# Optimization experiments

Hardware: AMD Instinct MI355X
Metric: run time of the kernel (lower is better)

Reference implementation:

```python
import jax, jax.numpy as jnp
from jax import lax
import numpy as np

B, T, NAG, MTASK = 8, 32, 50, 100  # batch, timesteps, n agents, m tasks
MTOP, NNB, L, H = 10, 10, 5, 512   # M top tasks, N neighbors (must equal M), L, hidden_dim
IN_DIM = NNB * MTOP * L + NNB * MTASK + NNB + NNB * MTOP  # 1610


def setup_inputs() -> dict:
    key = jax.random.key(0)
    ks = jax.random.split(key, 8)
    return {
        "beta": jax.random.normal(ks[0], (B, T, NAG, MTASK, L), dtype=jnp.float32),
        "actions_onehot": jax.random.uniform(ks[1], (B, T, NAG, MTASK), dtype=jnp.float32),
        "power_states": jax.random.normal(ks[2], (B, T, NAG), dtype=jnp.float32),
        "prev_assigns": jax.random.randint(ks[3], (B, T, NAG), 0, MTASK, dtype=jnp.int32),
        "W1": jax.random.normal(ks[4], (IN_DIM, H), dtype=jnp.float32) * 0.02,
        "b1": jnp.zeros((H,), jnp.float32),
        "W2": jax.random.normal(ks[5], (H, H), dtype=jnp.float32) * 0.02,
        "b2": jnp.zeros((H,), jnp.float32),
        "W3": jax.random.normal(ks[6], (H, MTOP + 1), dtype=jnp.float32) * 0.02,
        "b3": jnp.zeros((MTOP + 1,), jnp.float32),
    }


def _gather_agents(x, nb_flat):
    # x: [B,T,n,...]; nb_flat: [B,T,n*N] int -> [B,T,n,N,...]
    idx = nb_flat.reshape(B, T, NAG * NNB, *([1] * (x.ndim - 3)))
    out = jnp.take_along_axis(x, idx, axis=2)
    return out.reshape(B, T, NAG, NNB, *x.shape[3:])


def reference(beta, actions_onehot, power_states, prev_assigns, W1, b1, W2, b2, W3, b3):
    total_beta = beta.sum(-1)                              # [B,T,n,m]
    _, tasks = lax.top_k(total_beta, MTOP)                 # [B,T,n,M] top tasks per agent

    # benefit of agent a's best among agent i's top-M tasks: [B,T,i,a]
    tb_g = jnp.take_along_axis(total_beta, tasks.reshape(B, T, 1, NAG * MTOP), axis=3)
    best = tb_g.reshape(B, T, NAG, NAG, MTOP).max(-1)      # [B,T,a,i]
    best = best.transpose(0, 1, 3, 2)                      # [B,T,i,a]
    best = jnp.where(jnp.eye(NAG, dtype=bool), -jnp.inf, best)
    _, neighbors = lax.top_k(best, NNB)                    # [B,T,n,N]
    nb_flat = neighbors.reshape(B, T, NAG * NNB)

    # beta features: beta[b,t,nb(i,j),tasks(i,k),l] flattened in (M,N,L) order
    beta_nb = _gather_agents(beta, nb_flat)                # [B,T,n,N,m,L]
    beta_sel = jnp.take_along_axis(beta_nb, tasks[:, :, :, None, :, None], axis=4)  # [B,T,n,N,M,L]
    beta_feat = beta_sel.transpose(0, 1, 2, 4, 3, 5).reshape(B, T, NAG, NNB * MTOP * L)

    act_feat = _gather_agents(actions_onehot, nb_flat).reshape(B, T, NAG, NNB * MTASK)
    pow_feat = _gather_agents(power_states, nb_flat)       # [B,T,n,N]

    pa_nb = _gather_agents(prev_assigns, nb_flat)          # [B,T,n,N] int
    # one_hot(prev_assign)[task] == (prev_assign == task); flattened (M,N) order
    prev_feat = (tasks[:, :, :, :, None] == pa_nb[:, :, :, None, :]).astype(beta.dtype)
    prev_feat = prev_feat.reshape(B, T, NAG, MTOP * NNB)

    inputs = jnp.concatenate([beta_feat, act_feat, pow_feat, prev_feat], axis=-1)  # [B,T,n,1610]
    x = jax.nn.relu(inputs @ W1 + b1)
    x = jax.nn.relu(x @ W2 + b2)
    q = x @ W3 + b3                                        # [B,T,n,M+1]
    return q
```

## Files before the change

kernel.cpp:

```cpp
#include <hip/hip_runtime.h>
#include <math.h>

#define NB 8
#define NT 32
#define NAG 50
#define MTASK 100
#define MTOP 10
#define NNB 10
#define LDIM 5
#define HDIM 512
#define INDIM 1610
#define KP1 1664
#define NKT1 (KP1/32)
#define NKT2 (HDIM/32)
#define NROWS (NB*NT*NAG)
#define NOUT (MTOP+1)

typedef float f32x4 __attribute__((ext_vector_type(4)));
typedef _Float16 f16;
typedef _Float16 f16x8 __attribute__((ext_vector_type(8)));

__device__ __forceinline__ void gload16(const void* g, void* l) {
    __builtin_amdgcn_global_load_lds(
        (__attribute__((address_space(1))) void*)(g),
        (__attribute__((address_space(3))) void*)(l), 16, 0, 0);
}


__global__ __launch_bounds__(256) void k_topk(const float* __restrict__ beta,
                                              float* __restrict__ total_beta,
                                              int* __restrict__ tasks) {
    int wid = threadIdx.x >> 6, lane = threadIdx.x & 63;
    int row = blockIdx.x * 4 + wid;
    const float* bp = beta + (size_t)row * MTASK * LDIM;
    float v1, v2 = -INFINITY;
    {
        const float* p = bp + lane * LDIM;
        v1 = p[0] + p[1] + p[2] + p[3] + p[4];
        total_beta[(size_t)row * MTASK + lane] = v1;
    }
    if (lane + 64 < MTASK) {
        const float* p = bp + (lane + 64) * LDIM;
        v2 = p[0] + p[1] + p[2] + p[3] + p[4];
        total_beta[(size_t)row * MTASK + lane + 64] = v2;
    }
    for (int k = 0; k < MTOP; ++k) {
        float v; int idx;
        if (v1 >= v2) { v = v1; idx = lane; } else { v = v2; idx = lane + 64; }
        #pragma unroll
        for (int m = 1; m < 64; m <<= 1) {
            float vo = __shfl_xor(v, m, 64);
            int io = __shfl_xor(idx, m, 64);
            if (vo > v || (vo == v && io < idx)) { v = vo; idx = io; }
        }
        if (lane == 0) tasks[row * MTOP + k] = idx;
        if (idx == lane) v1 = -INFINITY;
        else if (idx == lane + 64) v2 = -INFINITY;
    }
}

__global__ __launch_bounds__(256) void k_nbrs(const float* __restrict__ total_beta,
                                              const int* __restrict__ tasks,
                                              int* __restrict__ neighbors) {
    int wid = threadIdx.x >> 6, lane = threadIdx.x & 63;
    int row = blockIdx.x * 4 + wid;
    int bt = row / NAG, i = row - bt * NAG;
    int tk[MTOP];
    #pragma unroll
    for (int k = 0; k < MTOP; ++k) tk[k] = tasks[row * MTOP + k];
    float v1 = -INFINITY;
    if (lane < NAG) {
        const float* tba = total_beta + ((size_t)bt * NAG + lane) * MTASK;
        float mx = -INFINITY;
        #pragma unroll
        for (int k = 0; k < MTOP; ++k) mx = fmaxf(mx, tba[tk[k]]);
        v1 = (lane == i) ? -INFINITY : mx;
    }
    for (int k = 0; k < NNB; ++k) {
        float v = v1; int idx = lane;
        #pragma unroll
        for (int m = 1; m < 64; m <<= 1) {
            float vo = __shfl_xor(v, m, 64);
            int io = __shfl_xor(idx, m, 64);
            if (vo > v || (vo == v && io < idx)) { v = vo; idx = io; }
        }
        if (lane == 0) neighbors[row * NNB + k] = idx;
        if (idx == lane) v1 = -INFINITY;
    }
}

__global__ __launch_bounds__(256) void k_build_inputs(
    const float* __restrict__ beta, const float* __restrict__ actions,
    const float* __restrict__ power, const int* __restrict__ prev,
    const int* __restrict__ tasks, const int* __restrict__ neighbors,
    f16* __restrict__ A) {
    int b = blockIdx.x;
    int t = threadIdx.x;
    __shared__ int tkv[8][MTOP], nbv[8][NNB], pav[8][NNB];
    __shared__ float pwv[8][NNB];
    __shared__ float fbuf[8][500];
    __shared__ float abuf[8][1004];
    if (t < 80) {
        int lr = t / 10, j = t - lr * 10;
        int row = b * 8 + lr;
        int bt = row / NAG;
        int nbj = neighbors[row * NNB + j];
        nbv[lr][j] = nbj;
        pav[lr][j] = prev[bt * NAG + nbj];
        pwv[lr][j] = power[bt * NAG + nbj];
        tkv[lr][j] = tasks[row * MTOP + j];
    }
    __syncthreads();
    int row0 = b * 8;
    #pragma unroll
    for (int it = 0; it < 4; ++it) {
        int idx = t + it * 256;
        if (idx < 800) {
            int l = idx / 100, p = idx - l * 100;
            int k = p / 10, j = p - k * 10;
            int row = row0 + l;
            int bt = row / NAG;
            const float* src = beta + ((size_t)(bt * NAG + nbv[l][j]) * MTASK
                                       + tkv[l][k]) * LDIM;
            int c0 = k * 50 + j * 5;
            #pragma unroll
            for (int i = 0; i < 5; ++i) fbuf[l][c0 + i] = src[i];
        }
    }
    #pragma unroll
    for (int it = 0; it < 8; ++it) {
        int idx = t + it * 256;
        if (idx < 2000) {
            int l = idx / 250, v = idx - l * 250;
            int j = v / 25, q = v - j * 25;
            int row = row0 + l;
            int bt = row / NAG;
            f32x4 a = *(const f32x4*)&actions[(size_t)(bt * NAG + nbv[l][j]) * MTASK + q * 4];
            *(f32x4*)&abuf[l][j * 100 + q * 4] = a;
        }
    }
    __syncthreads();
    int l = t & 7, og = t >> 3;
    int row = row0 + l;
    int rb = row >> 5, rlo = row & 31;
    #pragma unroll
    for (int s = 0; s < 7; ++s) {
        int o = og + 32 * s;
        if (o < 208) {
            f16 h8[8];
            #pragma unroll
            for (int e = 0; e < 8; ++e) {
                int c = o * 8 + e;
                float f;
                if (c < 500) {
                    f = fbuf[l][c];
                } else if (c < 1500) {
                    f = abuf[l][c - 500];
                } else if (c < 1510) {
                    f = pwv[l][c - 1500];
                } else if (c < 1610) {
                    int r2 = c - 1510, k = r2 / NNB, j = r2 - k * NNB;
                    f = (tkv[l][k] == pav[l][j]) ? 1.f : 0.f;
                } else {
                    f = 0.f;
                }
                h8[e] = (f16)f;
            }
            size_t off = ((size_t)rb * 208 + o) * 256 + rlo * 8;
            *(f16x8*)&A[off] = *(f16x8*)h8;
        }
    }
}

__global__ __launch_bounds__(256) void k_prep_wt(const float* __restrict__ W1,
                                                 const float* __restrict__ W2,
                                                 f16* __restrict__ T1,
                                                 f16* __restrict__ T2) {
    int bx = blockIdx.x, n0 = blockIdx.y * 64;
    const float* W; f16* T; int K, NKT, kp0;
    if (bx < KP1 / 64) { W = W1; T = T1; K = INDIM; NKT = NKT1; kp0 = bx * 64; }
    else               { W = W2; T = T2; K = HDIM;  NKT = NKT2; kp0 = (bx - KP1 / 64) * 64; }
    __shared__ float lds[64][65];
    int t = threadIdx.x;
    int cc = t & 63, r0 = t >> 6;
    #pragma unroll
    for (int i = 0; i < 16; ++i) {
        int rr = r0 + i * 4;
        int kp = kp0 + rr;
        lds[rr][cc] = (kp < K) ? W[(size_t)kp * HDIM + n0 + cc] : 0.f;
    }
    __syncthreads();
    int nblk = n0 >> 6;
    #pragma unroll
    for (int s = 0; s < 2; ++s) {
        int o = t + s * 256;
        int rn = o & 63, ko = o >> 6;
        int kp = kp0 + ko * 8;
        int kt = kp >> 5, kc = (kp >> 3) & 3;
        f16 h8[8];
        #pragma unroll
        for (int e = 0; e < 8; ++e) h8[e] = (f16)lds[ko * 8 + e][rn];
        size_t off = ((size_t)(nblk * NKT + kt) * 4 + kc) * 512 + rn * 8;
        *(f16x8*)&T[off] = *(f16x8*)h8;
    }
}

template<int NKT, int MODE>
__global__ __launch_bounds__(256, 4) void k_gemm(
    const f16* __restrict__ Ap, const f16* __restrict__ Bp,
    const float* __restrict__ bias, f16* __restrict__ C,
    const float* __restrict__ W3, float* __restrict__ qpart) {
    constexpr int SMEM = (MODE == 0) ? 20480 : 22528;
    __shared__ __align__(16) char smem[SMEM];
    f16* sA = (f16*)smem;
    f16* sB = (f16*)(smem + 4096);
    int tid = threadIdx.x, wid = tid >> 6, lane = tid & 63;
    int id = blockIdx.x;
    int swz = (id & 7) * 200 + (id >> 3);
    int nt = swz & 3, mt = swz >> 2;

    auto stage = [&](int kk, int buf) {
        #pragma unroll
        for (int j = 0; j < 3; ++j) {
            int seg = wid + 4 * j;
            if (seg < 2) {
                gload16(Ap + (size_t)(mt * NKT + kk) * 1024 + seg * 512 + lane * 8,
                        sA + buf * 1024 + seg * 512);
            } else if (seg < 10) {
                int s = seg - 2, q = s >> 2, kc = s & 3;
                gload16(Bp + ((size_t)((2 * nt + q) * NKT + kk) * 4 + kc) * 512 + lane * 8,
                        sB + buf * 4096 + (kc * 128 + q * 64) * 8);
            }
        }
    };

    int wr = wid >> 1, wc = wid & 1;
    int lrow = lane & 15, lk = lane >> 4;
    f32x4 acc[4] = {};

    stage(0, 0);
    for (int kk = 0; kk < NKT; ++kk) {
        int buf = kk & 1;
        __syncthreads();
        if (kk + 1 < NKT) stage(kk + 1, buf ^ 1);
        f16x8 a = *(const f16x8*)(sA + buf * 1024 + (lk * 32 + wr * 16 + lrow) * 8);
        f16x8 bh[4];
        #pragma unroll
        for (int j = 0; j < 4; ++j)
            bh[j] = *(const f16x8*)(sB + buf * 4096 + (lk * 128 + wc * 64 + j * 16 + lrow) * 8);
        #pragma unroll
        for (int j = 0; j < 4; ++j)
            acc[j] = __builtin_amdgcn_mfma_f32_16x16x32_f16(a, bh[j], acc[j], 0, 0, 0);
    }

    __syncthreads();
    float* sE = (float*)smem;
    #pragma unroll
    for (int j = 0; j < 4; ++j)
        #pragma unroll
        for (int r = 0; r < 4; ++r)
            sE[(wr * 16 + lk * 4 + r) * 132 + wc * 64 + j * 16 + lrow] = acc[j][r];

    if constexpr (MODE == 0) {
        __syncthreads();
        int l2 = tid & 31, og2 = tid >> 5;
        #pragma unroll
        for (int s2 = 0; s2 < 2; ++s2) {
            int o = og2 + 8 * s2;
            int n0 = nt * 128 + o * 8;
            f32x4 v0 = *(f32x4*)&sE[l2 * 132 + o * 8];
            f32x4 v1 = *(f32x4*)&sE[l2 * 132 + o * 8 + 4];
            f32x4 bb0 = *(const f32x4*)&bias[n0];
            f32x4 bb1 = *(const f32x4*)&bias[n0 + 4];
            f16 h8[8];
            #pragma unroll
            for (int i = 0; i < 4; ++i) {
                h8[i] = (f16)fmaxf(v0[i] + bb0[i], 0.f);
                h8[4 + i] = (f16)fmaxf(v1[i] + bb1[i], 0.f);
            }
            size_t off = ((size_t)mt * 64 + nt * 16 + o) * 256 + l2 * 8;
            *(f16x8*)&C[off] = *(f16x8*)h8;
        }
    } else {
        float* W3s = (float*)(smem + 16896);
        for (int i = tid; i < 128 * NOUT; i += 256)
            W3s[i] = W3[nt * 128 * NOUT + i];
        __syncthreads();
        int row = tid >> 3, seg = tid & 7;
        float a11[NOUT];
        #pragma unroll
        for (int n = 0; n < NOUT; ++n) a11[n] = 0.f;
        #pragma unroll
        for (int c16 = 0; c16 < 16; ++c16) {
            int col = seg + 8 * c16;
            float h = fmaxf(sE[row * 132 + col] + bias[nt * 128 + col], 0.f);
            const float* w = W3s + col * NOUT;
            #pragma unroll
            for (int n = 0; n < NOUT; ++n) a11[n] += h * w[n];
        }
        #pragma unroll
        for (int d = 4; d >= 1; d >>= 1)
            #pragma unroll
            for (int n = 0; n < NOUT; ++n) a11[n] += __shfl_down(a11[n], d, 64);
        if (seg == 0) {
            int grow = mt * 32 + row;
            #pragma unroll
            for (int n = 0; n < NOUT; ++n)
                qpart[(size_t)nt * NROWS * NOUT + (size_t)grow * NOUT + n] = a11[n];
        }
    }
}

__global__ __launch_bounds__(256) void k_qreduce(const float* __restrict__ qp,
                                                 const float* __restrict__ b3,
                                                 float* __restrict__ out) {
    int i = blockIdx.x * 256 + threadIdx.x;
    if (i < NROWS * NOUT) {
        int n = i % NOUT;
        const size_t P = (size_t)NROWS * NOUT;
        out[i] = b3[n] + qp[i] + qp[i + P] + qp[i + 2 * P] + qp[i + 3 * P];
    }
}

extern "C" void kernel_launch(void* const* d_in, const int* in_sizes, int n_in,
                              void* d_out, int out_size, void* d_ws, size_t ws_size,
                              hipStream_t stream) {
    const float* beta    = (const float*)d_in[0];
    const float* actions = (const float*)d_in[1];
    const float* power   = (const float*)d_in[2];
    const int*   prev    = (const int*)d_in[3];
    const float* W1      = (const float*)d_in[4];
    const float* b1      = (const float*)d_in[5];
    const float* W2      = (const float*)d_in[6];
    const float* b2      = (const float*)d_in[7];
    const float* W3      = (const float*)d_in[8];
    const float* b3      = (const float*)d_in[9];
    float* out = (float*)d_out;

    char* ws = (char*)d_ws;
    size_t off = 0;
    auto alloc = [&](size_t bytes) { void* p = ws + off; off += (bytes + 255) & ~(size_t)255; return p; };
    float* total_beta = (float*)alloc((size_t)NROWS * MTASK * 4);
    int*   tasks      = (int*)  alloc((size_t)NROWS * MTOP * 4);
    int*   neighbors  = (int*)  alloc((size_t)NROWS * NNB * 4);
    f16*   A    = (f16*)alloc((size_t)NROWS * KP1 * 2);
    f16*   W1t  = (f16*)alloc((size_t)HDIM * KP1 * 2);
    f16*   W2t  = (f16*)alloc((size_t)HDIM * HDIM * 2);
    f16*   h1   = (f16*)alloc((size_t)NROWS * HDIM * 2);
    float* qpart = (float*)alloc((size_t)4 * NROWS * NOUT * 4);

    k_topk<<<NROWS / 4, 256, 0, stream>>>(beta, total_beta, tasks);
    k_nbrs<<<NROWS / 4, 256, 0, stream>>>(total_beta, tasks, neighbors);
    k_build_inputs<<<NROWS / 8, 256, 0, stream>>>(beta, actions, power, prev, tasks,
                                                  neighbors, A);
    {
        dim3 gp(KP1 / 64 + HDIM / 64, HDIM / 64);
        k_prep_wt<<<gp, 256, 0, stream>>>(W1, W2, W1t, W2t);
    }
    k_gemm<NKT1, 0><<<1600, 256, 0, stream>>>(A, W1t, b1, h1, nullptr, nullptr);
    k_gemm<NKT2, 1><<<1600, 256, 0, stream>>>(h1, W2t, b2, nullptr, W3, qpart);
    k_qreduce<<<(NROWS * NOUT + 255) / 256, 256, 0, stream>>>(qpart, b3, out);
}
```

Baseline: 150.1 us.

## Fuse top-k and neighbor kernels per timestep; double GEMM M-tile to 64 rows

The per-row top-k and neighbor-selection kernels are merged into one kernel per (batch, timestep). It computes total_beta into shared memory, so the global total_beta buffer and one launch go away. The GEMM kernels now use 64-row M tiles instead of 32, with each wave computing two 16-row MFMA blocks. This means half as many blocks and better reuse of the staged B tile. The A and h1 layouts are changed to match. Shared memory per block grows, which may reduce occupancy, and the front kernel runs only 256 blocks.

Measured after the change: 180.3 us. +20.1%, slower.

```diff
diff --git a/kernel.cpp b/kernel.cpp
--- a/kernel.cpp
+++ b/kernel.cpp
@@ -27,65 +27,59 @@
 }
 
 
-__global__ __launch_bounds__(256) void k_topk(const float* __restrict__ beta,
-                                              float* __restrict__ total_beta,
-                                              int* __restrict__ tasks) {
-    int wid = threadIdx.x >> 6, lane = threadIdx.x & 63;
-    int row = blockIdx.x * 4 + wid;
-    const float* bp = beta + (size_t)row * MTASK * LDIM;
-    float v1, v2 = -INFINITY;
-    {
-        const float* p = bp + lane * LDIM;
-        v1 = p[0] + p[1] + p[2] + p[3] + p[4];
-        total_beta[(size_t)row * MTASK + lane] = v1;
-    }
-    if (lane + 64 < MTASK) {
-        const float* p = bp + (lane + 64) * LDIM;
-        v2 = p[0] + p[1] + p[2] + p[3] + p[4];
-        total_beta[(size_t)row * MTASK + lane + 64] = v2;
-    }
-    for (int k = 0; k < MTOP; ++k) {
-        float v; int idx;
-        if (v1 >= v2) { v = v1; idx = lane; } else { v = v2; idx = lane + 64; }
-        #pragma unroll
-        for (int m = 1; m < 64; m <<= 1) {
-            float vo = __shfl_xor(v, m, 64);
-            int io = __shfl_xor(idx, m, 64);
-            if (vo > v || (vo == v && io < idx)) { v = vo; idx = io; }
-        }
-        if (lane == 0) tasks[row * MTOP + k] = idx;
-        if (idx == lane) v1 = -INFINITY;
-        else if (idx == lane + 64) v2 = -INFINITY;
-    }
-}
-
-__global__ __launch_bounds__(256) void k_nbrs(const float* __restrict__ total_beta,
-                                              const int* __restrict__ tasks,
-                                              int* __restrict__ neighbors) {
-    int wid = threadIdx.x >> 6, lane = threadIdx.x & 63;
-    int row = blockIdx.x * 4 + wid;
-    int bt = row / NAG, i = row - bt * NAG;
-    int tk[MTOP];
-    #pragma unroll
-    for (int k = 0; k < MTOP; ++k) tk[k] = tasks[row * MTOP + k];
-    float v1 = -INFINITY;
-    if (lane < NAG) {
-        const float* tba = total_beta + ((size_t)bt * NAG + lane) * MTASK;
-        float mx = -INFINITY;
-        #pragma unroll
-        for (int k = 0; k < MTOP; ++k) mx = fmaxf(mx, tba[tk[k]]);
-        v1 = (lane == i) ? -INFINITY : mx;
-    }
-    for (int k = 0; k < NNB; ++k) {
-        float v = v1; int idx = lane;
-        #pragma unroll
-        for (int m = 1; m < 64; m <<= 1) {
-            float vo = __shfl_xor(v, m, 64);
-            int io = __shfl_xor(idx, m, 64);
-            if (vo > v || (vo == v && io < idx)) { v = vo; idx = io; }
-        }
-        if (lane == 0) neighbors[row * NNB + k] = idx;
-        if (idx == lane) v1 = -INFINITY;
+__global__ __launch_bounds__(512) void k_front(const float* __restrict__ beta,
+                                               int* __restrict__ tasks,
+                                               int* __restrict__ neighbors) {
+    int bt = blockIdx.x;
+    int t = threadIdx.x, wid = t >> 6, lane = t & 63;
+    __shared__ float tb[NAG][101];
+    __shared__ int   tk[NAG][MTOP];
+    const float* bsl = beta + (size_t)bt * NAG * MTASK * LDIM;
+    for (int i = t; i < NAG * MTASK; i += 512) {
+        const float* p = bsl + (size_t)i * LDIM;
+        tb[i / MTASK][i % MTASK] = p[0] + p[1] + p[2] + p[3] + p[4];
+    }
+    __syncthreads();
+    for (int row = wid; row < NAG; row += 8) {
+        float v1 = tb[row][lane];
+        float v2 = (lane + 64 < MTASK) ? tb[row][lane + 64] : -INFINITY;
+        for (int k = 0; k < MTOP; ++k) {
+            float v; int idx;
+            if (v1 >= v2) { v = v1; idx = lane; } else { v = v2; idx = lane + 64; }
+            #pragma unroll
+            for (int m = 1; m < 64; m <<= 1) {
+                float vo = __shfl_xor(v, m, 64);
+                int io = __shfl_xor(idx, m, 64);
+                if (vo > v || (vo == v && io < idx)) { v = vo; idx = io; }
+            }
+            if (lane == 0) {
+                tk[row][k] = idx;
+                tasks[(bt * NAG + row) * MTOP + k] = idx;
+            }
+            if (idx == lane) v1 = -INFINITY;
+            else if (idx == lane + 64) v2 = -INFINITY;
+        }
+    }
+    __syncthreads();
+    for (int row = wid; row < NAG; row += 8) {
+        float v1 = -INFINITY;
+        if (lane < NAG) {
+            float mx = -INFINITY;
+            #pragma unroll
+            for (int k = 0; k < MTOP; ++k) mx = fmaxf(mx, tb[lane][tk[row][k]]);
+            v1 = (lane == row) ? -INFINITY : mx;
+        }
+        for (int k = 0; k < NNB; ++k) {
+            float v = v1; int idx = lane;
+            #pragma unroll
+            for (int m = 1; m < 64; m <<= 1) {
+                float vo = __shfl_xor(v, m, 64);
+                int io = __shfl_xor(idx, m, 64);
+                if (vo > v || (vo == v && io < idx)) { v = vo; idx = io; }
+            }
+            if (lane == 0) neighbors[(bt * NAG + row) * NNB + k] = idx;
+            if (idx == lane) v1 = -INFINITY;
+        }
     }
 }
 
@@ -142,7 +136,7 @@
     __syncthreads();
     int l = t & 7, og = t >> 3;
     int row = row0 + l;
-    int rb = row >> 5, rlo = row & 31;
+    int rb = row >> 6, rlo = row & 63;
     #pragma unroll
     for (int s = 0; s < 7; ++s) {
         int o = og + 32 * s;
@@ -166,7 +160,7 @@
                 }
                 h8[e] = (f16)f;
             }
-            size_t off = ((size_t)rb * 208 + o) * 256 + rlo * 8;
+            size_t off = ((size_t)rb * 208 + o) * 512 + rlo * 8;
             *(f16x8*)&A[off] = *(f16x8*)h8;
         }
     }
@@ -210,24 +204,24 @@
     const f16* __restrict__ Ap, const f16* __restrict__ Bp,
     const float* __restrict__ bias, f16* __restrict__ C,
     const float* __restrict__ W3, float* __restrict__ qpart) {
-    constexpr int SMEM = (MODE == 0) ? 20480 : 22528;
+    constexpr int SMEM = (MODE == 0) ? 34048 : 39680;
     __shared__ __align__(16) char smem[SMEM];
     f16* sA = (f16*)smem;
-    f16* sB = (f16*)(smem + 4096);
+    f16* sB = (f16*)(smem + 8192);
     int tid = threadIdx.x, wid = tid >> 6, lane = tid & 63;
     int id = blockIdx.x;
-    int swz = (id & 7) * 200 + (id >> 3);
+    int swz = (id & 7) * 100 + (id >> 3);
     int nt = swz & 3, mt = swz >> 2;
 
     auto stage = [&](int kk, int buf) {
         #pragma unroll
         for (int j = 0; j < 3; ++j) {
             int seg = wid + 4 * j;
-            if (seg < 2) {
-                gload16(Ap + (size_t)(mt * NKT + kk) * 1024 + seg * 512 + lane * 8,
-                        sA + buf * 1024 + seg * 512);
-            } else if (seg < 10) {
-                int s = seg - 2, q = s >> 2, kc = s & 3;
+            if (seg < 4) {
+                gload16(Ap + ((size_t)(mt * NKT + kk) * 4 + seg) * 512 + lane * 8,
+                        sA + buf * 2048 + seg * 512);
+            } else {
+                int s = seg - 4, q = s >> 2, kc = s & 3;
                 gload16(Bp + ((size_t)((2 * nt + q) * NKT + kk) * 4 + kc) * 512 + lane * 8,
                         sB + buf * 4096 + (kc * 128 + q * 64) * 8);
             }
@@ -236,40 +230,46 @@
 
     int wr = wid >> 1, wc = wid & 1;
     int lrow = lane & 15, lk = lane >> 4;
-    f32x4 acc[4] = {};
+    f32x4 acc[2][4] = {};
 
     stage(0, 0);
     for (int kk = 0; kk < NKT; ++kk) {
         int buf = kk & 1;
         __syncthreads();
         if (kk + 1 < NKT) stage(kk + 1, buf ^ 1);
-        f16x8 a = *(const f16x8*)(sA + buf * 1024 + (lk * 32 + wr * 16 + lrow) * 8);
-        f16x8 bh[4];
+        f16x8 a[2], bh[4];
+        #pragma unroll
+        for (int i = 0; i < 2; ++i)
+            a[i] = *(const f16x8*)(sA + buf * 2048 + (lk * 64 + wr * 32 + i * 16 + lrow) * 8);
         #pragma unroll
         for (int j = 0; j < 4; ++j)
             bh[j] = *(const f16x8*)(sB + buf * 4096 + (lk * 128 + wc * 64 + j * 16 + lrow) * 8);
         #pragma unroll
+        for (int i = 0; i < 2; ++i)
+            #pragma unroll
+            for (int j = 0; j < 4; ++j)
+                acc[i][j] = __builtin_amdgcn_mfma_f32_16x16x32_f16(a[i], bh[j], acc[i][j], 0, 0, 0);
+    }
+
+    __syncthreads();
+    float* sE = (float*)smem;
+    #pragma unroll
+    for (int i = 0; i < 2; ++i)
+        #pragma unroll
         for (int j = 0; j < 4; ++j)
-            acc[j] = __builtin_amdgcn_mfma_f32_16x16x32_f16(a, bh[j], acc[j], 0, 0, 0);
-    }
-
-    __syncthreads();
-    float* sE = (float*)smem;
-    #pragma unroll
-    for (int j = 0; j < 4; ++j)
-        #pragma unroll
-        for (int r = 0; r < 4; ++r)
-            sE[(wr * 16 + lk * 4 + r) * 132 + wc * 64 + j * 16 + lrow] = acc[j][r];
+            #pragma unroll
+            for (int r = 0; r < 4; ++r)
+                sE[(wr * 32 + i * 16 + lk * 4 + r) * 133 + wc * 64 + j * 16 + lrow] = acc[i][j][r];
 
     if constexpr (MODE == 0) {
         __syncthreads();
-        int l2 = tid & 31, og2 = tid >> 5;
-        #pragma unroll
-        for (int s2 = 0; s2 < 2; ++s2) {
-            int o = og2 + 8 * s2;
+        int l2 = tid & 63, og2 = tid >> 6;
+        #pragma unroll
+        for (int s2 = 0; s2 < 4; ++s2) {
+            int o = og2 + 4 * s2;
             int n0 = nt * 128 + o * 8;
-            f32x4 v0 = *(f32x4*)&sE[l2 * 132 + o * 8];
-            f32x4 v1 = *(f32x4*)&sE[l2 * 132 + o * 8 + 4];
+            f32x4 v0 = *(f32x4*)&sE[l2 * 133 + o * 8];
+            f32x4 v1 = *(f32x4*)&sE[l2 * 133 + o * 8 + 4];
             f32x4 bb0 = *(const f32x4*)&bias[n0];
             f32x4 bb1 = *(const f32x4*)&bias[n0 + 4];
             f16 h8[8];
@@ -278,32 +278,32 @@
                 h8[i] = (f16)fmaxf(v0[i] + bb0[i], 0.f);
                 h8[4 + i] = (f16)fmaxf(v1[i] + bb1[i], 0.f);
             }
-            size_t off = ((size_t)mt * 64 + nt * 16 + o) * 256 + l2 * 8;
+            size_t off = ((size_t)mt * 64 + nt * 16 + o) * 512 + l2 * 8;
             *(f16x8*)&C[off] = *(f16x8*)h8;
         }
     } else {
-        float* W3s = (float*)(smem + 16896);
+        float* W3s = (float*)(smem + 34048);
         for (int i = tid; i < 128 * NOUT; i += 256)
             W3s[i] = W3[nt * 128 * NOUT + i];
         __syncthreads();
-        int row = tid >> 3, seg = tid & 7;
+        int row = tid >> 2, seg = tid & 3;
         float a11[NOUT];
         #pragma unroll
         for (int n = 0; n < NOUT; ++n) a11[n] = 0.f;
         #pragma unroll
-        for (int c16 = 0; c16 < 16; ++c16) {
-            int col = seg + 8 * c16;
-            float h = fmaxf(sE[row * 132 + col] + bias[nt * 128 + col], 0.f);
+        for (int c32 = 0; c32 < 32; ++c32) {
+            int col = seg + 4 * c32;
+            float h = fmaxf(sE[row * 133 + col] + bias[nt * 128 + col], 0.f);
             const float* w = W3s + col * NOUT;
             #pragma unroll
             for (int n = 0; n < NOUT; ++n) a11[n] += h * w[n];
         }
         #pragma unroll
-        for (int d = 4; d >= 1; d >>= 1)
+        for (int d = 2; d >= 1; d >>= 1)
             #pragma unroll
             for (int n = 0; n < NOUT; ++n) a11[n] += __shfl_down(a11[n], d, 64);
         if (seg == 0) {
-            int grow = mt * 32 + row;
+            int grow = mt * 64 + row;
             #pragma unroll
             for (int n = 0; n < NOUT; ++n)
                 qpart[(size_t)nt * NROWS * NOUT + (size_t)grow * NOUT + n] = a11[n];
@@ -340,24 +340,22 @@
     char* ws = (char*)d_ws;
     size_t off = 0;
     auto alloc = [&](size_t bytes) { void* p = ws + off; off += (bytes + 255) & ~(size_t)255; return p; };
-    float* total_beta = (float*)alloc((size_t)NROWS * MTASK * 4);
-    int*   tasks      = (int*)  alloc((size_t)NROWS * MTOP * 4);
-    int*   neighbors  = (int*)  alloc((size_t)NROWS * NNB * 4);
+    int*   tasks     = (int*)alloc((size_t)NROWS * MTOP * 4);
+    int*   neighbors = (int*)alloc((size_t)NROWS * NNB * 4);
     f16*   A    = (f16*)alloc((size_t)NROWS * KP1 * 2);
     f16*   W1t  = (f16*)alloc((size_t)HDIM * KP1 * 2);
     f16*   W2t  = (f16*)alloc((size_t)HDIM * HDIM * 2);
     f16*   h1   = (f16*)alloc((size_t)NROWS * HDIM * 2);
     float* qpart = (float*)alloc((size_t)4 * NROWS * NOUT * 4);
 
-    k_topk<<<NROWS / 4, 256, 0, stream>>>(beta, total_beta, tasks);
-    k_nbrs<<<NROWS / 4, 256, 0, stream>>>(total_beta, tasks, neighbors);
+    k_front<<<NB * NT, 512, 0, stream>>>(beta, tasks, neighbors);
     k_build_inputs<<<NROWS / 8, 256, 0, stream>>>(beta, actions, power, prev, tasks,
                                                   neighbors, A);
     {
         dim3 gp(KP1 / 64 + HDIM / 64, HDIM / 64);
         k_prep_wt<<<gp, 256, 0, stream>>>(W1, W2, W1t, W2t);
     }
-    k_gemm<NKT1, 0><<<1600, 256, 0, stream>>>(A, W1t, b1, h1, nullptr, nullptr);
-    k_gemm<NKT2, 1><<<1600, 256, 0, stream>>>(h1, W2t, b2, nullptr, W3, qpart);
+    k_gemm<NKT1, 0><<<800, 256, 0, stream>>>(A, W1t, b1, h1, nullptr, nullptr);
+    k_gemm<NKT2, 1><<<800, 256, 0, stream>>>(h1, W2t, b2, nullptr, W3, qpart);
     k_qreduce<<<(NROWS * NOUT + 255) / 256, 256, 0, stream>>>(qpart, b3, out);
 }
```
